# Kernel tuning notes

Hardware: AMD Instinct MI355X
Metric: run time of the kernel (lower is better)

Reference implementation:

```python
import jax, jax.numpy as jnp
import numpy as np

EMB = 768
HEADS = 8
HEAD_DIM = EMB // HEADS  # 96
B, N = 4, 2048


def setup_inputs() -> dict:
    key = jax.random.key(0)
    ks = jax.random.split(key, 9)
    s = 1.0 / np.sqrt(EMB)
    x = jax.random.normal(ks[0], (B, N, EMB), dtype=jnp.float32)
    Wq = jax.random.uniform(ks[1], (EMB, EMB), jnp.float32, -s, s)
    bq = jax.random.uniform(ks[2], (EMB,), jnp.float32, -s, s)
    Wk = jax.random.uniform(ks[3], (EMB, EMB), jnp.float32, -s, s)
    bk = jax.random.uniform(ks[4], (EMB,), jnp.float32, -s, s)
    Wv = jax.random.uniform(ks[5], (EMB, EMB), jnp.float32, -s, s)
    bv = jax.random.uniform(ks[6], (EMB,), jnp.float32, -s, s)
    Wo = jax.random.uniform(ks[7], (EMB, EMB), jnp.float32, -s, s)
    bo = jax.random.uniform(ks[8], (EMB,), jnp.float32, -s, s)
    return {"x": x, "Wq": Wq, "bq": bq, "Wk": Wk, "bk": bk,
            "Wv": Wv, "bv": bv, "Wo": Wo, "bo": bo}


def _split_heads(t):
    b, n, _ = t.shape
    return t.reshape(b, n, HEADS, HEAD_DIM).transpose(0, 2, 1, 3)  # b h n d


def reference(x, Wq, bq, Wk, bk, Wv, bv, Wo, bo):
    q = _split_heads(x @ Wq + bq)
    k = _split_heads(x @ Wk + bk)
    v = _split_heads(x @ Wv + bv)
    # NOTE: faithful to source — softmax on UNSCALED logits, then divide by sqrt(head_dim)
    energy = jnp.einsum('bhqd,bhkd->bhqk', q, k)
    att = jax.nn.softmax(energy, axis=-1) / np.sqrt(HEAD_DIM)
    out = jnp.einsum('bhqk,bhkd->bhqd', att, v)
    out = out.transpose(0, 2, 1, 3).reshape(x.shape[0], x.shape[1], EMB)
    return out @ Wo + bo
```

## Files before the change

kernel.cpp:

```cpp
#include <hip/hip_runtime.h>

typedef _Float16 half_t;
typedef __attribute__((ext_vector_type(8))) _Float16 half8;
typedef __attribute__((ext_vector_type(2))) __fp16 fp16x2;
typedef __attribute__((ext_vector_type(4))) float f32x4;
typedef __attribute__((ext_vector_type(16))) float f32x16;

#define EMB 768
#define HEADS 8
#define HD 96
#define BB 4
#define NN 2048
#define BN (BB*NN)

static __device__ __forceinline__ f32x4 mfma16(half8 a, half8 b, f32x4 c) {
    return __builtin_amdgcn_mfma_f32_16x16x32_f16(a, b, c, 0, 0, 0);
}
static __device__ __forceinline__ f32x16 mfma32(half8 a, half8 b, f32x16 c) {
    return __builtin_amdgcn_mfma_f32_32x32x16_f16(a, b, c, 0, 0, 0);
}
static __device__ __forceinline__ unsigned pkrtz(float a, float b) {
    fp16x2 h = __builtin_amdgcn_cvt_pkrtz(a, b);
    return __builtin_bit_cast(unsigned, h);
}
static __device__ __forceinline__ unsigned sx32(unsigned v) {
    return (unsigned)__shfl_xor((int)v, 32);
}

__global__ void cvt_f32_f16(const float* __restrict__ in, half_t* __restrict__ out, int n4) {
    int i = blockIdx.x * blockDim.x + threadIdx.x;
    if (i < n4) {
        float4 v = ((const float4*)in)[i];
        union { half_t h[4]; uint2 u; } t;
        t.h[0] = (half_t)v.x; t.h[1] = (half_t)v.y;
        t.h[2] = (half_t)v.z; t.h[3] = (half_t)v.w;
        ((uint2*)out)[i] = t.u;
    }
}

__global__ __launch_bounds__(256) void cvt_transpose_w(
    const float* __restrict__ W0, const float* __restrict__ W1,
    const float* __restrict__ W2, const float* __restrict__ W3,
    half_t* __restrict__ T0, half_t* __restrict__ T1,
    half_t* __restrict__ T2, half_t* __restrict__ T3)
{
    const float* W; half_t* T;
    switch (blockIdx.z) {
        case 0: W = W0; T = T0; break;
        case 1: W = W1; T = T1; break;
        case 2: W = W2; T = T2; break;
        default: W = W3; T = T3; break;
    }
    __shared__ float ls[32][33];
    const int k0 = blockIdx.x * 32, n0 = blockIdx.y * 32;
    const int r = threadIdx.x >> 3, c4 = (threadIdx.x & 7) * 4;
    float4 v = *(const float4*)&W[(size_t)(k0 + r) * EMB + n0 + c4];
    ls[r][c4+0] = v.x; ls[r][c4+1] = v.y; ls[r][c4+2] = v.z; ls[r][c4+3] = v.w;
    __syncthreads();
    union { half_t h[4]; uint2 u; } t;
    #pragma unroll
    for (int j = 0; j < 4; ++j) t.h[j] = (half_t)ls[c4 + j][r];
    *(uint2*)&T[(size_t)(n0 + r) * EMB + k0 + c4] = t.u;
}

__global__ __launch_bounds__(256) void proj_qkv_h(
    const half_t* __restrict__ xh,
    const half_t* __restrict__ WqT, const float* __restrict__ bq,
    const half_t* __restrict__ WkT, const float* __restrict__ bk,
    const half_t* __restrict__ WvT, const float* __restrict__ bv,
    half_t* __restrict__ Qo, half_t* __restrict__ Ko, half_t* __restrict__ Vt)
{
    const half_t* WT; const float* bias;
    const int z = blockIdx.z;
    if (z == 0)      { WT = WqT; bias = bq; }
    else if (z == 1) { WT = WkT; bias = bk; }
    else             { WT = WvT; bias = bv; }

    __shared__ half_t As[128][56];
    __shared__ half_t Bs[128][56];

    const int tid = threadIdx.x;
    const int lane = tid & 63;
    const int wid = tid >> 6;
    const int lr = lane & 15;
    const int lkg = lane >> 4;
    const int wm = (wid >> 1) * 64;
    const int wn = (wid & 1) * 64;
    const int mbase = blockIdx.x * 128;
    const int nbase = blockIdx.y * 128;

    const int srr = tid >> 2;
    const int skk = (tid & 3) * 8;

    f32x4 acc[4][4];
    const f32x4 z4 = {0.f, 0.f, 0.f, 0.f};
    #pragma unroll
    for (int i = 0; i < 4; ++i)
        #pragma unroll
        for (int j = 0; j < 4; ++j) acc[i][j] = z4;

    const half_t* aptr = xh + (size_t)(mbase + srr) * EMB + skk;
    const half_t* bptr = WT + (size_t)(nbase + srr) * EMB + skk;

    half8 a0 = *(const half8*)aptr;
    half8 a1 = *(const half8*)(aptr + 64 * EMB);
    half8 b0 = *(const half8*)bptr;
    half8 b1 = *(const half8*)(bptr + 64 * EMB);

    for (int k0 = 0; k0 < EMB; k0 += 32) {
        __syncthreads();
        *(half8*)&As[srr][skk]      = a0;
        *(half8*)&As[srr + 64][skk] = a1;
        *(half8*)&Bs[srr][skk]      = b0;
        *(half8*)&Bs[srr + 64][skk] = b1;
        __syncthreads();
        if (k0 + 32 < EMB) {
            a0 = *(const half8*)(aptr + k0 + 32);
            a1 = *(const half8*)(aptr + k0 + 32 + 64 * EMB);
            b0 = *(const half8*)(bptr + k0 + 32);
            b1 = *(const half8*)(bptr + k0 + 32 + 64 * EMB);
        }
        half8 af[4], bf[4];
        #pragma unroll
        for (int mi = 0; mi < 4; ++mi)
            af[mi] = *(const half8*)&As[wm + mi*16 + lr][lkg*8];
        #pragma unroll
        for (int ni = 0; ni < 4; ++ni)
            bf[ni] = *(const half8*)&Bs[wn + ni*16 + lr][lkg*8];
        #pragma unroll
        for (int mi = 0; mi < 4; ++mi)
            #pragma unroll
            for (int ni = 0; ni < 4; ++ni)
                acc[mi][ni] = mfma16(af[mi], bf[ni], acc[mi][ni]);
    }

    const float qscale = (z == 0) ? 1.4426950408889634f : 1.0f;

    #pragma unroll
    for (int ni = 0; ni < 4; ++ni) {
        const int e = nbase + wn + ni*16 + lr;
        const float be = bias[e];
        const int h = e / HD, d = e % HD;
        #pragma unroll
        for (int mi = 0; mi < 4; ++mi) {
            const int row0 = mbase + wm + mi*16 + lkg*4;
            const int b = row0 >> 11, n0 = row0 & (NN - 1);
            if (z == 2) {
                union { half_t hh[4]; uint2 u; } t;
                #pragma unroll
                for (int r = 0; r < 4; ++r) t.hh[r] = (half_t)(acc[mi][ni][r] + be);
                *(uint2*)&Vt[((size_t)(b*HEADS + h) * HD + d) * NN + n0] = t.u;
            } else {
                half_t* outp = (z == 0) ? Qo : Ko;
                #pragma unroll
                for (int r = 0; r < 4; ++r)
                    outp[((size_t)(b*HEADS + h) * NN + n0 + r) * HD + d] =
                        (half_t)((acc[mi][ni][r] + be) * qscale);
            }
        }
    }
}

__global__ __launch_bounds__(256, 3) void attn_h(
    const half_t* __restrict__ Qh, const half_t* __restrict__ Kh,
    const half_t* __restrict__ Vth, half_t* __restrict__ AOh)
{
    __shared__ __align__(16) char smem[24576];

    const int tid = threadIdx.x;
    const int lane = tid & 63;
    const int wid = tid >> 6;
    const int l31 = lane & 31;
    const int b5 = lane >> 5;
    const int wq = wid * 32;
    const int qbase = blockIdx.x * 128;
    const int bh = blockIdx.y;

    const half_t* Qp = Qh + (size_t)bh * NN * HD;
    const half_t* Kp = Kh + (size_t)bh * NN * HD;
    const half_t* Vp = Vth + (size_t)bh * HD * NN;
    half_t* AOp = AOh + (size_t)bh * NN * HD;

    const int kr = tid >> 2;
    const int kcb = (tid & 3) * 48;
    const int vd = tid >> 1;
    const int vcb = (tid & 1) * 64;
    half8 kv0, kv1, kv2, vv0, vv1, vv2, vv3;
    {
        const half_t* ksrc = Kp + (size_t)kr * HD + kcb / 2;
        kv0 = *(const half8*)(ksrc);
        kv1 = *(const half8*)(ksrc + 8);
        kv2 = *(const half8*)(ksrc + 16);
        if (tid < 192) {
            const half_t* vsrc = Vp + (size_t)vd * NN + vcb / 2;
            vv0 = *(const half8*)(vsrc);      vv1 = *(const half8*)(vsrc + 8);
            vv2 = *(const half8*)(vsrc + 16); vv3 = *(const half8*)(vsrc + 24);
        }
    }

    {
        const int r = tid >> 1;
        const int cb = (tid & 1) * 96;
        const half_t* src = Qp + (size_t)(qbase + r) * HD + cb / 2;
        #pragma unroll
        for (int c = 0; c < 6; ++c) {
            half8 q = *(const half8*)(src + c * 8);
            *(half8*)(smem + ((r * 192 + cb + c * 16) ^ ((r & 7) << 4))) = q;
        }
    }
    __syncthreads();
    half8 qf[6];
    {
        const int r = wq + l31;
        #pragma unroll
        for (int kg = 0; kg < 6; ++kg)
            qf[kg] = *(const half8*)(smem + ((r * 192 + kg * 32 + 16 * b5) ^ ((r & 7) << 4)));
    }
    __syncthreads();

    f32x16 acc[3];
    const f32x16 z16 = {0.f,0.f,0.f,0.f,0.f,0.f,0.f,0.f,0.f,0.f,0.f,0.f,0.f,0.f,0.f,0.f};
    acc[0] = z16; acc[1] = z16; acc[2] = z16;
    float mreg = -1e30f, lreg = 0.f;

    for (int kt = 0; kt < NN / 64; ++kt) {
        {
            *(half8*)((char*)smem + ((kr * 192 + kcb +  0) ^ ((kr & 7) << 4))) = kv0;
            *(half8*)((char*)smem + ((kr * 192 + kcb + 16) ^ ((kr & 7) << 4))) = kv1;
            *(half8*)((char*)smem + ((kr * 192 + kcb + 32) ^ ((kr & 7) << 4))) = kv2;
            if (tid < 192) {
                char* vb = smem + 12288;
                *(half8*)(vb + ((vd * 128 + vcb +  0) ^ ((vd & 7) << 4))) = vv0;
                *(half8*)(vb + ((vd * 128 + vcb + 16) ^ ((vd & 7) << 4))) = vv1;
                *(half8*)(vb + ((vd * 128 + vcb + 32) ^ ((vd & 7) << 4))) = vv2;
                *(half8*)(vb + ((vd * 128 + vcb + 48) ^ ((vd & 7) << 4))) = vv3;
            }
        }
        __syncthreads();

        if (kt + 1 < NN / 64) {
            const int kb = (kt + 1) * 64;
            const half_t* ksrc = Kp + (size_t)(kb + kr) * HD + kcb / 2;
            kv0 = *(const half8*)(ksrc);
            kv1 = *(const half8*)(ksrc + 8);
            kv2 = *(const half8*)(ksrc + 16);
            if (tid < 192) {
                const half_t* vsrc = Vp + (size_t)vd * NN + kb + vcb / 2;
                vv0 = *(const half8*)(vsrc);      vv1 = *(const half8*)(vsrc + 8);
                vv2 = *(const half8*)(vsrc + 16); vv3 = *(const half8*)(vsrc + 24);
            }
        }

        #pragma unroll
        for (int tile = 0; tile < 2; ++tile) {
            f32x16 st = z16;
            #pragma unroll
            for (int kg = 0; kg < 6; ++kg) {
                const int kv = tile * 32 + l31;
                half8 kf = *(const half8*)(smem +
                    ((kv * 192 + kg * 32 + 16 * b5) ^ ((kv & 7) << 4)));
                st = mfma32(kf, qf[kg], st);
            }

            float tm = st[0];
            #pragma unroll
            for (int i = 1; i < 16; ++i) tm = fmaxf(tm, st[i]);
            tm = fmaxf(tm, __shfl_xor(tm, 32));

            if (!__all(tm <= mreg + 8.0f)) {
                const float mn = fmaxf(mreg, tm);
                const float sc = exp2f(mreg - mn);
                lreg *= sc;
                #pragma unroll
                for (int db = 0; db < 3; ++db)
                    #pragma unroll
                    for (int i = 0; i < 16; ++i) acc[db][i] *= sc;
                mreg = mn;
            }

            float rs = 0.f;
            #pragma unroll
            for (int i = 0; i < 16; ++i) {
                const float p = exp2f(st[i] - mreg);
                st[i] = p;
                rs += p;
            }
            rs += __shfl_xor(rs, 32);
            lreg += rs;

            unsigned pk[4][2];
            #pragma unroll
            for (int rr = 0; rr < 4; ++rr) {
                pk[rr][0] = pkrtz(st[rr*4+0], st[rr*4+1]);
                pk[rr][1] = pkrtz(st[rr*4+2], st[rr*4+3]);
            }

            #pragma unroll
            for (int ks = 0; ks < 2; ++ks) {
                const unsigned z0 = b5 ? pk[2*ks][0] : pk[2*ks+1][0];
                const unsigned z1 = b5 ? pk[2*ks][1] : pk[2*ks+1][1];
                const unsigned x0 = sx32(z0);
                const unsigned x1 = sx32(z1);
                union { unsigned u[4]; half8 h; } afu;
                afu.u[0] = b5 ? x0 : pk[2*ks][0];
                afu.u[1] = b5 ? x1 : pk[2*ks][1];
                afu.u[2] = b5 ? pk[2*ks+1][0] : x0;
                afu.u[3] = b5 ? pk[2*ks+1][1] : x1;
                const half8 af = afu.h;
                #pragma unroll
                for (int db = 0; db < 3; ++db) {
                    const int d = db * 32 + l31;
                    half8 vf = *(const half8*)(smem + 12288 +
                        ((d * 128 + tile * 64 + ks * 32 + 16 * b5) ^ ((d & 7) << 4)));
                    acc[db] = mfma32(vf, af, acc[db]);
                }
            }
        }
        __syncthreads();
    }

    const float isq = 0.10206207261596577f;
    const float inv = isq / lreg;
    const int q = qbase + wq + l31;
    half_t* dst = AOp + (size_t)q * HD;
    #pragma unroll
    for (int db = 0; db < 3; ++db)
        #pragma unroll
        for (int rr = 0; rr < 4; ++rr) {
            const int d0 = db * 32 + rr * 8 + 4 * b5;
            union { half_t h[4]; uint2 u; } t;
            #pragma unroll
            for (int r = 0; r < 4; ++r)
                t.h[r] = (half_t)(acc[db][rr*4 + r] * inv);
            *(uint2*)&dst[d0] = t.u;
        }
}

__global__ __launch_bounds__(256) void proj_out_h(
    const half_t* __restrict__ AOh, const half_t* __restrict__ WoT,
    const float* __restrict__ bo, float* __restrict__ out)
{
    __shared__ half_t As[128][56];
    __shared__ half_t Bs[128][56];

    const int tid = threadIdx.x;
    const int lane = tid & 63;
    const int wid = tid >> 6;
    const int lr = lane & 15;
    const int lkg = lane >> 4;
    const int wm = (wid >> 1) * 64;
    const int wn = (wid & 1) * 64;
    const int mbase = blockIdx.x * 128;
    const int nbase = blockIdx.y * 128;

    const int srr = tid >> 2;
    const int skk = (tid & 3) * 8;

    const int arow0 = mbase + srr;
    const int ab0 = arow0 >> 11, an0 = arow0 & (NN - 1);
    const int arow1 = arow0 + 64;
    const int ab1 = arow1 >> 11, an1 = arow1 & (NN - 1);

    f32x4 acc[4][4];
    const f32x4 z4 = {0.f, 0.f, 0.f, 0.f};
    #pragma unroll
    for (int i = 0; i < 4; ++i)
        #pragma unroll
        for (int j = 0; j < 4; ++j) acc[i][j] = z4;

    const half_t* bptr = WoT + (size_t)(nbase + srr) * EMB + skk;

#define ALOAD(b_, n_, k0_) \
    (*(const half8*)&AOh[((size_t)((b_)*HEADS + (k0_)/HD) * NN + (n_)) * HD + ((k0_)%HD) + skk])

    half8 a0 = ALOAD(ab0, an0, 0);
    half8 a1 = ALOAD(ab1, an1, 0);
    half8 b0 = *(const half8*)bptr;
    half8 b1 = *(const half8*)(bptr + 64 * EMB);

    for (int k0 = 0; k0 < EMB; k0 += 32) {
        __syncthreads();
        *(half8*)&As[srr][skk]      = a0;
        *(half8*)&As[srr + 64][skk] = a1;
        *(half8*)&Bs[srr][skk]      = b0;
        *(half8*)&Bs[srr + 64][skk] = b1;
        __syncthreads();
        if (k0 + 32 < EMB) {
            const int kn = k0 + 32;
            a0 = ALOAD(ab0, an0, kn);
            a1 = ALOAD(ab1, an1, kn);
            b0 = *(const half8*)(bptr + kn);
            b1 = *(const half8*)(bptr + kn + 64 * EMB);
        }
        half8 af[4], bf[4];
        #pragma unroll
        for (int mi = 0; mi < 4; ++mi)
            af[mi] = *(const half8*)&As[wm + mi*16 + lr][lkg*8];
        #pragma unroll
        for (int ni = 0; ni < 4; ++ni)
            bf[ni] = *(const half8*)&Bs[wn + ni*16 + lr][lkg*8];
        #pragma unroll
        for (int mi = 0; mi < 4; ++mi)
            #pragma unroll
            for (int ni = 0; ni < 4; ++ni)
                acc[mi][ni] = mfma16(af[mi], bf[ni], acc[mi][ni]);
    }
#undef ALOAD

    #pragma unroll
    for (int ni = 0; ni < 4; ++ni) {
        const int e = nbase + wn + ni*16 + lr;
        const float be = bo[e];
        #pragma unroll
        for (int mi = 0; mi < 4; ++mi) {
            const int row0 = mbase + wm + mi*16 + lkg*4;
            #pragma unroll
            for (int r = 0; r < 4; ++r)
                out[(size_t)(row0 + r) * EMB + e] = acc[mi][ni][r] + be;
        }
    }
}

extern "C" void kernel_launch(void* const* d_in, const int* in_sizes, int n_in,
                              void* d_out, int out_size, void* d_ws, size_t ws_size,
                              hipStream_t stream)
{
    const float* x  = (const float*)d_in[0];
    const float* Wq = (const float*)d_in[1];
    const float* bq = (const float*)d_in[2];
    const float* Wk = (const float*)d_in[3];
    const float* bk = (const float*)d_in[4];
    const float* Wv = (const float*)d_in[5];
    const float* bv = (const float*)d_in[6];
    const float* Wo = (const float*)d_in[7];
    const float* bo = (const float*)d_in[8];

    const size_t SZ = (size_t)BN * EMB;
    const size_t WS = (size_t)EMB * EMB;

    half_t* ws  = (half_t*)d_ws;
    half_t* xh  = ws;
    half_t* WqT = xh  + SZ;
    half_t* WkT = WqT + WS;
    half_t* WvT = WkT + WS;
    half_t* WoT = WvT + WS;
    half_t* Qh  = WoT + WS;
    half_t* Kh  = Qh  + SZ;
    half_t* Vth = Kh  + SZ;
    half_t* AOh = Vth + SZ;

    cvt_f32_f16<<<(int)(SZ / 4 / 256), 256, 0, stream>>>(x, xh, (int)(SZ / 4));
    cvt_transpose_w<<<dim3(EMB/32, EMB/32, 4), 256, 0, stream>>>(
        Wq, Wk, Wv, Wo, WqT, WkT, WvT, WoT);

    proj_qkv_h<<<dim3(BN/128, EMB/128, 3), 256, 0, stream>>>(
        xh, WqT, bq, WkT, bk, WvT, bv, Qh, Kh, Vth);

    attn_h<<<dim3(NN/128, BB*HEADS), 256, 0, stream>>>(Qh, Kh, Vth, AOh);

    proj_out_h<<<dim3(BN/128, EMB/128), 256, 0, stream>>>(AOh, WoT, bo, (float*)d_out);
}
```

Measured before the change: 169.9 us.

## Split KV tiles across warps in attention and fuse x conversion into QKV GEMM

The attention kernel now handles 64 queries per block instead of 128. The two warp pairs each process half of every 64-key tile, and their partial softmax states (max, sum, accumulator) are merged through shared memory at the end. This doubles the grid and raises occupancy (launch bounds 4). The separate fp32-to-fp16 conversion kernel for x is removed. The QKV projection now loads fp32 x directly and packs it to fp16 in registers, saving one launch and a round-trip of x through memory. In exchange, each attention block re-reads K/V for fewer queries, there is extra reduction work in the epilogue, and the QKV GEMM issues twice the global load bytes for its A operand.

```diff
diff --git a/kernel.cpp b/kernel.cpp
--- a/kernel.cpp
+++ b/kernel.cpp
@@ -26,16 +26,11 @@
 static __device__ __forceinline__ unsigned sx32(unsigned v) {
     return (unsigned)__shfl_xor((int)v, 32);
 }
-
-__global__ void cvt_f32_f16(const float* __restrict__ in, half_t* __restrict__ out, int n4) {
-    int i = blockIdx.x * blockDim.x + threadIdx.x;
-    if (i < n4) {
-        float4 v = ((const float4*)in)[i];
-        union { half_t h[4]; uint2 u; } t;
-        t.h[0] = (half_t)v.x; t.h[1] = (half_t)v.y;
-        t.h[2] = (half_t)v.z; t.h[3] = (half_t)v.w;
-        ((uint2*)out)[i] = t.u;
-    }
+static __device__ __forceinline__ half8 pack8(float4 a, float4 b) {
+    union { unsigned u[4]; half8 h; } t;
+    t.u[0] = pkrtz(a.x, a.y); t.u[1] = pkrtz(a.z, a.w);
+    t.u[2] = pkrtz(b.x, b.y); t.u[3] = pkrtz(b.z, b.w);
+    return t.h;
 }
 
 __global__ __launch_bounds__(256) void cvt_transpose_w(
@@ -64,7 +59,7 @@
 }
 
 __global__ __launch_bounds__(256) void proj_qkv_h(
-    const half_t* __restrict__ xh,
+    const float* __restrict__ x,
     const half_t* __restrict__ WqT, const float* __restrict__ bq,
     const half_t* __restrict__ WkT, const float* __restrict__ bk,
     const half_t* __restrict__ WvT, const float* __restrict__ bv,
@@ -99,11 +94,13 @@
         #pragma unroll
         for (int j = 0; j < 4; ++j) acc[i][j] = z4;
 
-    const half_t* aptr = xh + (size_t)(mbase + srr) * EMB + skk;
+    const float*  aptr = x  + (size_t)(mbase + srr) * EMB + skk;
     const half_t* bptr = WT + (size_t)(nbase + srr) * EMB + skk;
 
-    half8 a0 = *(const half8*)aptr;
-    half8 a1 = *(const half8*)(aptr + 64 * EMB);
+    half8 a0 = pack8(*(const float4*)(aptr),
+                     *(const float4*)(aptr + 4));
+    half8 a1 = pack8(*(const float4*)(aptr + 64 * EMB),
+                     *(const float4*)(aptr + 64 * EMB + 4));
     half8 b0 = *(const half8*)bptr;
     half8 b1 = *(const half8*)(bptr + 64 * EMB);
 
@@ -115,8 +112,10 @@
         *(half8*)&Bs[srr + 64][skk] = b1;
         __syncthreads();
         if (k0 + 32 < EMB) {
-            a0 = *(const half8*)(aptr + k0 + 32);
-            a1 = *(const half8*)(aptr + k0 + 32 + 64 * EMB);
+            a0 = pack8(*(const float4*)(aptr + k0 + 32),
+                       *(const float4*)(aptr + k0 + 36));
+            a1 = pack8(*(const float4*)(aptr + k0 + 32 + 64 * EMB),
+                       *(const float4*)(aptr + k0 + 36 + 64 * EMB));
             b0 = *(const half8*)(bptr + k0 + 32);
             b1 = *(const half8*)(bptr + k0 + 32 + 64 * EMB);
         }
@@ -161,19 +160,20 @@
     }
 }
 
-__global__ __launch_bounds__(256, 3) void attn_h(
+__global__ __launch_bounds__(256, 4) void attn_h(
     const half_t* __restrict__ Qh, const half_t* __restrict__ Kh,
     const half_t* __restrict__ Vth, half_t* __restrict__ AOh)
 {
-    __shared__ __align__(16) char smem[24576];
+    __shared__ __align__(16) char smem[25088];
 
     const int tid = threadIdx.x;
     const int lane = tid & 63;
     const int wid = tid >> 6;
     const int l31 = lane & 31;
     const int b5 = lane >> 5;
-    const int wq = wid * 32;
-    const int qbase = blockIdx.x * 128;
+    const int qsub = wid & 1;
+    const int sub = wid >> 1;
+    const int qbase = blockIdx.x * 64;
     const int bh = blockIdx.y;
 
     const half_t* Qp = Qh + (size_t)bh * NN * HD;
@@ -199,11 +199,11 @@
     }
 
     {
-        const int r = tid >> 1;
-        const int cb = (tid & 1) * 96;
+        const int r = tid >> 2;
+        const int cb = (tid & 3) * 48;
         const half_t* src = Qp + (size_t)(qbase + r) * HD + cb / 2;
         #pragma unroll
-        for (int c = 0; c < 6; ++c) {
+        for (int c = 0; c < 3; ++c) {
             half8 q = *(const half8*)(src + c * 8);
             *(half8*)(smem + ((r * 192 + cb + c * 16) ^ ((r & 7) << 4))) = q;
         }
@@ -211,7 +211,7 @@
     __syncthreads();
     half8 qf[6];
     {
-        const int r = wq + l31;
+        const int r = qsub * 32 + l31;
         #pragma unroll
         for (int kg = 0; kg < 6; ++kg)
             qf[kg] = *(const half8*)(smem + ((r * 192 + kg * 32 + 16 * b5) ^ ((r & 7) << 4)));
@@ -223,18 +223,18 @@
     acc[0] = z16; acc[1] = z16; acc[2] = z16;
     float mreg = -1e30f, lreg = 0.f;
 
+    const int kvrow = sub * 32 + l31;
+
     for (int kt = 0; kt < NN / 64; ++kt) {
-        {
-            *(half8*)((char*)smem + ((kr * 192 + kcb +  0) ^ ((kr & 7) << 4))) = kv0;
-            *(half8*)((char*)smem + ((kr * 192 + kcb + 16) ^ ((kr & 7) << 4))) = kv1;
-            *(half8*)((char*)smem + ((kr * 192 + kcb + 32) ^ ((kr & 7) << 4))) = kv2;
-            if (tid < 192) {
-                char* vb = smem + 12288;
-                *(half8*)(vb + ((vd * 128 + vcb +  0) ^ ((vd & 7) << 4))) = vv0;
-                *(half8*)(vb + ((vd * 128 + vcb + 16) ^ ((vd & 7) << 4))) = vv1;
-                *(half8*)(vb + ((vd * 128 + vcb + 32) ^ ((vd & 7) << 4))) = vv2;
-                *(half8*)(vb + ((vd * 128 + vcb + 48) ^ ((vd & 7) << 4))) = vv3;
-            }
+        *(half8*)(smem + ((kr * 192 + kcb +  0) ^ ((kr & 7) << 4))) = kv0;
+        *(half8*)(smem + ((kr * 192 + kcb + 16) ^ ((kr & 7) << 4))) = kv1;
+        *(half8*)(smem + ((kr * 192 + kcb + 32) ^ ((kr & 7) << 4))) = kv2;
+        if (tid < 192) {
+            char* vb = smem + 12288;
+            *(half8*)(vb + ((vd * 128 + vcb +  0) ^ ((vd & 7) << 4))) = vv0;
+            *(half8*)(vb + ((vd * 128 + vcb + 16) ^ ((vd & 7) << 4))) = vv1;
+            *(half8*)(vb + ((vd * 128 + vcb + 32) ^ ((vd & 7) << 4))) = vv2;
+            *(half8*)(vb + ((vd * 128 + vcb + 48) ^ ((vd & 7) << 4))) = vv3;
         }
         __syncthreads();
 
@@ -251,89 +251,106 @@
             }
         }
 
-        #pragma unroll
-        for (int tile = 0; tile < 2; ++tile) {
-            f32x16 st = z16;
-            #pragma unroll
-            for (int kg = 0; kg < 6; ++kg) {
-                const int kv = tile * 32 + l31;
-                half8 kf = *(const half8*)(smem +
-                    ((kv * 192 + kg * 32 + 16 * b5) ^ ((kv & 7) << 4)));
-                st = mfma32(kf, qf[kg], st);
+        f32x16 st = z16;
+        #pragma unroll
+        for (int kg = 0; kg < 6; ++kg) {
+            half8 kf = *(const half8*)(smem +
+                ((kvrow * 192 + kg * 32 + 16 * b5) ^ ((kvrow & 7) << 4)));
+            st = mfma32(kf, qf[kg], st);
+        }
+
+        float tm = st[0];
+        #pragma unroll
+        for (int i = 1; i < 16; ++i) tm = fmaxf(tm, st[i]);
+        tm = fmaxf(tm, __shfl_xor(tm, 32));
+
+        if (!__all(tm <= mreg + 8.0f)) {
+            const float mn = fmaxf(mreg, tm);
+            const float sc = exp2f(mreg - mn);
+            lreg *= sc;
+            #pragma unroll
+            for (int db = 0; db < 3; ++db)
+                #pragma unroll
+                for (int i = 0; i < 16; ++i) acc[db][i] *= sc;
+            mreg = mn;
+        }
+
+        float rs = 0.f;
+        #pragma unroll
+        for (int i = 0; i < 16; ++i) {
+            const float p = exp2f(st[i] - mreg);
+            st[i] = p;
+            rs += p;
+        }
+        rs += __shfl_xor(rs, 32);
+        lreg += rs;
+
+        unsigned pk[4][2];
+        #pragma unroll
+        for (int rr = 0; rr < 4; ++rr) {
+            pk[rr][0] = pkrtz(st[rr*4+0], st[rr*4+1]);
+            pk[rr][1] = pkrtz(st[rr*4+2], st[rr*4+3]);
+        }
+
+        #pragma unroll
+        for (int ks = 0; ks < 2; ++ks) {
+            const unsigned z0 = b5 ? pk[2*ks][0] : pk[2*ks+1][0];
+            const unsigned z1 = b5 ? pk[2*ks][1] : pk[2*ks+1][1];
+            const unsigned x0 = sx32(z0);
+            const unsigned x1 = sx32(z1);
+            union { unsigned u[4]; half8 h; } afu;
+            afu.u[0] = b5 ? x0 : pk[2*ks][0];
+            afu.u[1] = b5 ? x1 : pk[2*ks][1];
+            afu.u[2] = b5 ? pk[2*ks+1][0] : x0;
+            afu.u[3] = b5 ? pk[2*ks+1][1] : x1;
+            const half8 af = afu.h;
+            #pragma unroll
+            for (int db = 0; db < 3; ++db) {
+                const int d = db * 32 + l31;
+                half8 vf = *(const half8*)(smem + 12288 +
+                    ((d * 128 + sub * 64 + ks * 32 + 16 * b5) ^ ((d & 7) << 4)));
+                acc[db] = mfma32(vf, af, acc[db]);
             }
-
-            float tm = st[0];
-            #pragma unroll
-            for (int i = 1; i < 16; ++i) tm = fmaxf(tm, st[i]);
-            tm = fmaxf(tm, __shfl_xor(tm, 32));
-
-            if (!__all(tm <= mreg + 8.0f)) {
-                const float mn = fmaxf(mreg, tm);
-                const float sc = exp2f(mreg - mn);
-                lreg *= sc;
+        }
+        __syncthreads();
+    }
+
+    float* fb = (float*)smem;
+    fb[tid] = mreg;
+    fb[256 + tid] = lreg;
+    __syncthreads();
+    const float mp = fb[tid ^ 128];
+    const float lp = fb[256 + (tid ^ 128)];
+    const float mc = fmaxf(mreg, mp);
+    const float sc = exp2f(mreg - mc);
+    const float lc = lreg * sc + lp * exp2f(mp - mc);
+    __syncthreads();
+    if (wid >= 2) {
+        float* rec = fb + (qsub * 64 + lane) * 49;
+        #pragma unroll
+        for (int db = 0; db < 3; ++db)
+            #pragma unroll
+            for (int i = 0; i < 16; ++i) rec[db*16 + i] = acc[db][i] * sc;
+    }
+    __syncthreads();
+    if (wid < 2) {
+        const float* rec = fb + (qsub * 64 + lane) * 49;
+        const float isq = 0.10206207261596577f;
+        const float inv = isq / lc;
+        const int q = qbase + qsub * 32 + l31;
+        half_t* dst = AOp + (size_t)q * HD;
+        #pragma unroll
+        for (int db = 0; db < 3; ++db)
+            #pragma unroll
+            for (int rr = 0; rr < 4; ++rr) {
+                const int d0 = db * 32 + rr * 8 + 4 * b5;
+                union { half_t h[4]; uint2 u; } t;
                 #pragma unroll
-                for (int db = 0; db < 3; ++db)
-                    #pragma unroll
-                    for (int i = 0; i < 16; ++i) acc[db][i] *= sc;
-                mreg = mn;
+                for (int r = 0; r < 4; ++r)
+                    t.h[r] = (half_t)((acc[db][rr*4 + r] * sc + rec[db*16 + rr*4 + r]) * inv);
+                *(uint2*)&dst[d0] = t.u;
             }
-
-            float rs = 0.f;
-            #pragma unroll
-            for (int i = 0; i < 16; ++i) {
-                const float p = exp2f(st[i] - mreg);
-                st[i] = p;
-                rs += p;
-            }
-            rs += __shfl_xor(rs, 32);
-            lreg += rs;
-
-            unsigned pk[4][2];
-            #pragma unroll
-            for (int rr = 0; rr < 4; ++rr) {
-                pk[rr][0] = pkrtz(st[rr*4+0], st[rr*4+1]);
-                pk[rr][1] = pkrtz(st[rr*4+2], st[rr*4+3]);
-            }
-
-            #pragma unroll
-            for (int ks = 0; ks < 2; ++ks) {
-                const unsigned z0 = b5 ? pk[2*ks][0] : pk[2*ks+1][0];
-                const unsigned z1 = b5 ? pk[2*ks][1] : pk[2*ks+1][1];
-                const unsigned x0 = sx32(z0);
-                const unsigned x1 = sx32(z1);
-                union { unsigned u[4]; half8 h; } afu;
-                afu.u[0] = b5 ? x0 : pk[2*ks][0];
-                afu.u[1] = b5 ? x1 : pk[2*ks][1];
-                afu.u[2] = b5 ? pk[2*ks+1][0] : x0;
-                afu.u[3] = b5 ? pk[2*ks+1][1] : x1;
-                const half8 af = afu.h;
-                #pragma unroll
-                for (int db = 0; db < 3; ++db) {
-                    const int d = db * 32 + l31;
-                    half8 vf = *(const half8*)(smem + 12288 +
-                        ((d * 128 + tile * 64 + ks * 32 + 16 * b5) ^ ((d & 7) << 4)));
-                    acc[db] = mfma32(vf, af, acc[db]);
-                }
-            }
-        }
-        __syncthreads();
-    }
-
-    const float isq = 0.10206207261596577f;
-    const float inv = isq / lreg;
-    const int q = qbase + wq + l31;
-    half_t* dst = AOp + (size_t)q * HD;
-    #pragma unroll
-    for (int db = 0; db < 3; ++db)
-        #pragma unroll
-        for (int rr = 0; rr < 4; ++rr) {
-            const int d0 = db * 32 + rr * 8 + 4 * b5;
-            union { half_t h[4]; uint2 u; } t;
-            #pragma unroll
-            for (int r = 0; r < 4; ++r)
-                t.h[r] = (half_t)(acc[db][rr*4 + r] * inv);
-            *(uint2*)&dst[d0] = t.u;
-        }
+    }
 }
 
 __global__ __launch_bounds__(256) void proj_out_h(
@@ -439,8 +456,7 @@
     const size_t WS = (size_t)EMB * EMB;
 
     half_t* ws  = (half_t*)d_ws;
-    half_t* xh  = ws;
-    half_t* WqT = xh  + SZ;
+    half_t* WqT = ws;
     half_t* WkT = WqT + WS;
     half_t* WvT = WkT + WS;
     half_t* WoT = WvT + WS;
@@ -449,14 +465,13 @@
     half_t* Vth = Kh  + SZ;
     half_t* AOh = Vth + SZ;
 
-    cvt_f32_f16<<<(int)(SZ / 4 / 256), 256, 0, stream>>>(x, xh, (int)(SZ / 4));
     cvt_transpose_w<<<dim3(EMB/32, EMB/32, 4), 256, 0, stream>>>(
         Wq, Wk, Wv, Wo, WqT, WkT, WvT, WoT);
 
     proj_qkv_h<<<dim3(BN/128, EMB/128, 3), 256, 0, stream>>>(
-        xh, WqT, bq, WkT, bk, WvT, bv, Qh, Kh, Vth);
-
-    attn_h<<<dim3(NN/128, BB*HEADS), 256, 0, stream>>>(Qh, Kh, Vth, AOh);
+        x, WqT, bq, WkT, bk, WvT, bv, Qh, Kh, Vth);
+
+    attn_h<<<dim3(NN/64, BB*HEADS), 256, 0, stream>>>(Qh, Kh, Vth, AOh);
 
     proj_out_h<<<dim3(BN/128, EMB/128), 256, 0, stream>>>(AOh, WoT, bo, (float*)d_out);
 }
```

Result: slower. 233.5 us (+37.4%).
